# Kernel optimization log

Measured on AMD Instinct MI355X. Metric: run time of the kernel, lower is better.

The kernel has to match this reference:

```python
import jax, jax.numpy as jnp
import numpy as np
from jax.scipy.special import erf

N = 4096        # n_points
M = 65536       # number of interaction events
T_MAX = 100.0   # observation window end
BETA0 = 1.0


def setup_inputs() -> dict:
    key = jax.random.key(0)
    k1, k2, k3, k4 = jax.random.split(key, 4)
    # data columns: [node_i, node_j, time] (indices stored as floats, as in the torch code)
    ij = jax.random.randint(k1, (M, 2), 0, N).astype(jnp.float32)
    times = jax.random.uniform(k2, (M,), minval=0.0, maxval=T_MAX)
    data = jnp.concatenate([ij, times[:, None]], axis=1)
    # learned parameters, initialized like the torch module
    z0 = jax.random.uniform(k3, (N, 2), dtype=jnp.float32) * 0.5
    v0 = jax.random.uniform(k4, (N, 2), dtype=jnp.float32) * 0.5
    beta = jnp.full((1, 1), BETA0, dtype=jnp.float32)
    t0 = jnp.float32(0.0)
    tn = jnp.float32(T_MAX)
    return {"data": data, "t0": t0, "tn": tn, "beta": beta, "z0": z0, "v0": v0}


def reference(data, t0, tn, beta, z0, v0):
    b = beta[0, 0]
    times = data[:, 2]                                   # (M,)
    i = jnp.floor(data[:, 0]).astype(jnp.int32)          # (M,)
    j = jnp.floor(data[:, 1]).astype(jnp.int32)          # (M,)

    # --- event term: log lambda_ij(t) = beta - ||z_i(t) - z_j(t)||^2, gathered per event.
    # (Identical to building the dense [N,N,M] tensor and fancy-indexing it.)
    zi = z0[i] + v0[i] * times[:, None]                  # (M,2)
    zj = z0[j] + v0[j] * times[:, None]                  # (M,2)
    d_event = jnp.sum((zi - zj) ** 2, axis=1)            # (M,)
    event_intensity = jnp.sum(b - d_event)

    # --- non-event term: closed-form integral of exp(beta - ||dz + dv*t||^2) over [t0, tn]
    # ||dz + dv t||^2 = a t^2 + bb t + c with a=|dv|^2, bb=2 dz.dv, c=|dz|^2
    dz = z0[:, None, :] - z0[None, :, :]                 # (N,N,2)
    dv = v0[:, None, :] - v0[None, :, :]                 # (N,N,2)
    a = jnp.sum(dv * dv, axis=-1)                        # (N,N)
    bb = 2.0 * jnp.sum(dz * dv, axis=-1)                 # (N,N)
    c = jnp.sum(dz * dz, axis=-1)                        # (N,N)
    a_safe = jnp.maximum(a, 1e-10)
    sqa = jnp.sqrt(a_safe)
    # exponent beta - (c - bb^2/(4a)) <= beta, numerically safe
    pref = (jnp.sqrt(jnp.pi) / (2.0 * sqa)) * jnp.exp(b + bb * bb / (4.0 * a_safe) - c)
    upper = erf(sqa * tn + bb / (2.0 * sqa))
    lower = erf(sqa * t0 + bb / (2.0 * sqa))
    integral = pref * (upper - lower)                    # (N,N)
    triu_mask = jnp.triu(jnp.ones((N, N), dtype=bool), k=1)
    non_event_intensity = jnp.sum(jnp.where(triu_mask, integral, 0.0))

    return event_intensity - non_event_intensity
```

## Files before the change

### kernel.cpp

```cpp
#include <hip/hip_runtime.h>


__device__ __forceinline__ float fast_erf(float x) {
    const float ax = __builtin_fabsf(x);
    const float t  = __builtin_amdgcn_rcpf(fmaf(0.3275911f, ax, 1.0f));
    float p = fmaf(t, 1.061405429f, -1.453152027f);
    p = fmaf(t, p, 1.421413741f);
    p = fmaf(t, p, -0.284496736f);
    p = fmaf(t, p, 0.254829592f);
    const float y = fmaf(-t * p, __expf(-ax * ax), 1.0f);
    return __builtin_copysignf(y, x);
}

__device__ __forceinline__ float erf_small(float x) {
    const float x2 = x * x;
    float p = fmaf(x2, 0.0052239776f, -0.0268661706f);
    p = fmaf(x2, p, 0.1128379167f);
    p = fmaf(x2, p, -0.3761263890f);
    p = fmaf(x2, p, 1.1283791671f);
    return x * p;
}

template<bool T0Z>
__device__ __forceinline__ float pair_rows(int r0, int r1, int jofs, int N,
                                           const float2* __restrict__ z2,
                                           const float2* __restrict__ v2,
                                           float t0, float tn, float b) {
    const float SQRT_PI_OVER_2 = 0.88622692545275801f;
    float acc = 0.0f;
    #pragma unroll
    for (int r = 0; r < 2; ++r) {
        const int i = (r == 0) ? r0 : r1;
        if (r == 1 && r1 == r0) break;
        const float2 zi = z2[i];
        const float2 vi = v2[i];
        #pragma unroll 4
        for (int j = i + 1 + jofs; j < N; j += 512) {
            const float2 zj = z2[j];
            const float2 vj = v2[j];
            const float dzx = zi.x - zj.x, dzy = zi.y - zj.y;
            const float dvx = vi.x - vj.x, dvy = vi.y - vj.y;

            const float a  = fmaf(dvx, dvx, dvy * dvy);
            const float du = fmaf(dzx, dvx, dzy * dvy);
            const float c  = fmaf(dzx, dzx, dzy * dzy);

            const float a_safe = fmaxf(a, 1e-10f);
            const float rsq = __builtin_amdgcn_rsqf(a_safe);
            const float sqa = a_safe * rsq;
            const float u   = du * rsq;

            const float pref  = SQRT_PI_OVER_2 * rsq * __expf(fmaf(u, u, b - c));
            const float upper = fast_erf(fmaf(sqa, tn, u));
            const float lower = T0Z ? erf_small(u)
                                    : fast_erf(fmaf(sqa, t0, u));
            acc += pref * (upper - lower);
        }
    }
    return acc;
}

__device__ __forceinline__ float block_reduce_add(float v) {
    __shared__ float smem[16];
    #pragma unroll
    for (int off = 32; off > 0; off >>= 1)
        v += __shfl_down(v, off, 64);
    const int lane = threadIdx.x & 63;
    const int wave = threadIdx.x >> 6;
    if (lane == 0) smem[wave] = v;
    __syncthreads();
    if (threadIdx.x == 0) {
        float s = smem[0];
        const int nw = (int)blockDim.x >> 6;
        for (int w = 1; w < nw; ++w) s += smem[w];
        return s;
    }
    return 0.0f;
}

__global__ void __launch_bounds__(256)
fused_kernel(const float* __restrict__ data,
             const float* __restrict__ t0p,
             const float* __restrict__ tnp,
             const float* __restrict__ beta,
             const float* __restrict__ z0,
             const float* __restrict__ v0,
             float* __restrict__ ws, int M, int N) {
    const float t0 = t0p[0];
    const float tn = tnp[0];
    const float b  = beta[0];
    const float2* __restrict__ z2 = (const float2*)z0;
    const float2* __restrict__ v2 = (const float2*)v0;

    float acc = 0.0f;

    const int gstride = gridDim.x * blockDim.x;
    for (int m = blockIdx.x * blockDim.x + threadIdx.x; m < M; m += gstride) {
        const float fi = data[3 * m + 0];
        const float fj = data[3 * m + 1];
        const float t  = data[3 * m + 2];
        const int ii = (int)fi;
        const int jj = (int)fj;
        const float2 zi = z2[ii], zj = z2[jj];
        const float2 vi = v2[ii], vj = v2[jj];
        const float dx = (zi.x - zj.x) + (vi.x - vj.x) * t;
        const float dy = (zi.y - zj.y) + (vi.y - vj.y) * t;
        acc += b - (dx * dx + dy * dy);
    }

    const int pair = (int)blockIdx.x >> 1;
    const int half = (int)blockIdx.x & 1;
    const int r0 = pair;
    const int r1 = N - 1 - pair;
    const int jofs = (half << 8) + (int)threadIdx.x;

    float psum;
    if (t0 == 0.0f)
        psum = pair_rows<true >(r0, r1, jofs, N, z2, v2, t0, tn, b);
    else
        psum = pair_rows<false>(r0, r1, jofs, N, z2, v2, t0, tn, b);
    acc -= psum;

    const float s = block_reduce_add(acc);
    if (threadIdx.x == 0) ws[blockIdx.x] = s;
}

__global__ void __launch_bounds__(1024)
finalize_kernel(const float* __restrict__ ws, float* __restrict__ out,
                int nblocks) {
    const float4* __restrict__ ws4 = (const float4*)ws;
    const int n4 = nblocks >> 2;
    float v = 0.0f;
    for (int k = threadIdx.x; k < n4; k += 1024) {
        const float4 p = ws4[k];
        v += (p.x + p.y) + (p.z + p.w);
    }
    const float s = block_reduce_add(v);
    if (threadIdx.x == 0) out[0] = s;
}

extern "C" void kernel_launch(void* const* d_in, const int* in_sizes, int n_in,
                              void* d_out, int out_size, void* d_ws, size_t ws_size,
                              hipStream_t stream) {
    const float* data = (const float*)d_in[0];
    const float* t0   = (const float*)d_in[1];
    const float* tn   = (const float*)d_in[2];
    const float* beta = (const float*)d_in[3];
    const float* z0   = (const float*)d_in[4];
    const float* v0   = (const float*)d_in[5];
    float* out = (float*)d_out;
    float* ws  = (float*)d_ws;

    const int M = in_sizes[0] / 3;
    const int N = in_sizes[4] / 2;

    const int blocks = 2 * ((N + 1) / 2);
    fused_kernel<<<blocks, 256, 0, stream>>>(data, t0, tn, beta, z0, v0, ws, M, N);
    finalize_kernel<<<1, 1024, 0, stream>>>(ws, out, blocks);
}
```

Measured before the change: 79.24 us.

## Use exp-free rational erf for upper bound and halve grid with full-row blocks

```diff
diff --git a/kernel.cpp b/kernel.cpp
--- a/kernel.cpp
+++ b/kernel.cpp
@@ -1,7 +1,7 @@
 #include <hip/hip_runtime.h>
 
 
-__device__ __forceinline__ float fast_erf(float x) {
+__device__ __forceinline__ float fast_erf_a(float x) {
     const float ax = __builtin_fabsf(x);
     const float t  = __builtin_amdgcn_rcpf(fmaf(0.3275911f, ax, 1.0f));
     float p = fmaf(t, 1.061405429f, -1.453152027f);
@@ -9,6 +9,18 @@
     p = fmaf(t, p, -0.284496736f);
     p = fmaf(t, p, 0.254829592f);
     const float y = fmaf(-t * p, __expf(-ax * ax), 1.0f);
+    return __builtin_copysignf(y, x);
+}
+
+__device__ __forceinline__ float fast_erf_b(float x) {
+    const float ax = __builtin_fabsf(x);
+    float p = fmaf(ax, 0.078108f, 0.000972f);
+    p = fmaf(ax, p, 0.230389f);
+    p = fmaf(ax, p, 0.278393f);
+    p = fmaf(ax, p, 1.0f);
+    const float w  = __builtin_amdgcn_rcpf(p);
+    const float w2 = w * w;
+    const float y  = fmaf(-w2, w2, 1.0f);
     return __builtin_copysignf(y, x);
 }
 
@@ -22,7 +34,7 @@
 }
 
 template<bool T0Z>
-__device__ __forceinline__ float pair_rows(int r0, int r1, int jofs, int N,
+__device__ __forceinline__ float pair_rows(int r0, int r1, int N,
                                            const float2* __restrict__ z2,
                                            const float2* __restrict__ v2,
                                            float t0, float tn, float b) {
@@ -35,7 +47,7 @@
         const float2 zi = z2[i];
         const float2 vi = v2[i];
         #pragma unroll 4
-        for (int j = i + 1 + jofs; j < N; j += 512) {
+        for (int j = i + 1 + (int)threadIdx.x; j < N; j += 256) {
             const float2 zj = z2[j];
             const float2 vj = v2[j];
             const float dzx = zi.x - zj.x, dzy = zi.y - zj.y;
@@ -51,9 +63,9 @@
             const float u   = du * rsq;
 
             const float pref  = SQRT_PI_OVER_2 * rsq * __expf(fmaf(u, u, b - c));
-            const float upper = fast_erf(fmaf(sqa, tn, u));
+            const float upper = fast_erf_b(fmaf(sqa, tn, u));
             const float lower = T0Z ? erf_small(u)
-                                    : fast_erf(fmaf(sqa, t0, u));
+                                    : fast_erf_a(fmaf(sqa, t0, u));
             acc += pref * (upper - lower);
         }
     }
@@ -94,8 +106,10 @@
 
     float acc = 0.0f;
 
-    const int gstride = gridDim.x * blockDim.x;
-    for (int m = blockIdx.x * blockDim.x + threadIdx.x; m < M; m += gstride) {
+    const int chunk  = (M + (int)gridDim.x - 1) / (int)gridDim.x;
+    const int mbeg   = (int)blockIdx.x * chunk;
+    const int mend   = min(mbeg + chunk, M);
+    for (int m = mbeg + (int)threadIdx.x; m < mend; m += 256) {
         const float fi = data[3 * m + 0];
         const float fj = data[3 * m + 1];
         const float t  = data[3 * m + 2];
@@ -108,17 +122,14 @@
         acc += b - (dx * dx + dy * dy);
     }
 
-    const int pair = (int)blockIdx.x >> 1;
-    const int half = (int)blockIdx.x & 1;
-    const int r0 = pair;
-    const int r1 = N - 1 - pair;
-    const int jofs = (half << 8) + (int)threadIdx.x;
+    const int r0 = (int)blockIdx.x;
+    const int r1 = N - 1 - r0;
 
     float psum;
     if (t0 == 0.0f)
-        psum = pair_rows<true >(r0, r1, jofs, N, z2, v2, t0, tn, b);
+        psum = pair_rows<true >(r0, r1, N, z2, v2, t0, tn, b);
     else
-        psum = pair_rows<false>(r0, r1, jofs, N, z2, v2, t0, tn, b);
+        psum = pair_rows<false>(r0, r1, N, z2, v2, t0, tn, b);
     acc -= psum;
 
     const float s = block_reduce_add(acc);
@@ -135,6 +146,8 @@
         const float4 p = ws4[k];
         v += (p.x + p.y) + (p.z + p.w);
     }
+    if (threadIdx.x == 0)
+        for (int k = n4 << 2; k < nblocks; ++k) v += ws[k];
     const float s = block_reduce_add(v);
     if (threadIdx.x == 0) out[0] = s;
 }
@@ -154,7 +167,7 @@
     const int M = in_sizes[0] / 3;
     const int N = in_sizes[4] / 2;
 
-    const int blocks = 2 * ((N + 1) / 2);
+    const int blocks = (N + 1) / 2;
     fused_kernel<<<blocks, 256, 0, stream>>>(data, t0, tn, beta, z0, v0, ws, M, N);
     finalize_kernel<<<1, 1024, 0, stream>>>(ws, out, blocks);
 }
```

Measured after the change: 77.96 us. Within noise of the previous version (-1.6%).
